# Optimization experiments

Hardware: AMD Instinct MI355X
Metric: run time of the kernel (lower is better)

Reference implementation:

```python
import jax, jax.numpy as jnp
import numpy as np

N = 50000      # nodes
E = 800000     # edges (before self-loops)
F_IN = 128     # num_features
HID = 32       # hidden_channels
HEADS = 4
CLS = 40       # num_classes
NEG_SLOPE = 0.2


def setup_inputs() -> dict:
    key = jax.random.key(0)
    ks = jax.random.split(key, 10)
    s = 0.1
    x = jax.random.normal(ks[0], (N, F_IN), jnp.float32)
    edge_index = jax.random.randint(ks[1], (2, E), 0, N, jnp.int32)
    W1 = jax.random.normal(ks[2], (F_IN, HEADS * HID), jnp.float32) * s
    att_src1 = jax.random.normal(ks[3], (HEADS, HID), jnp.float32) * s
    att_dst1 = jax.random.normal(ks[4], (HEADS, HID), jnp.float32) * s
    b1 = jnp.zeros((HEADS * HID,), jnp.float32)
    W2 = jax.random.normal(ks[5], (HEADS * HID, CLS), jnp.float32) * s
    att_src2 = jax.random.normal(ks[6], (1, CLS), jnp.float32) * s
    att_dst2 = jax.random.normal(ks[7], (1, CLS), jnp.float32) * s
    b2 = jnp.zeros((CLS,), jnp.float32)
    return {"x": x, "edge_index": edge_index,
            "W1": W1, "att_src1": att_src1, "att_dst1": att_dst1, "b1": b1,
            "W2": W2, "att_src2": att_src2, "att_dst2": att_dst2, "b2": b2}


def gat_layer(x, src, dst, W, a_src, a_dst, b, concat):
    """PyG GATConv: per-head linear, edge attention logits a_src.h_j + a_dst.h_i,
    LeakyReLU, segment softmax over incoming edges per dst, weighted scatter-sum."""
    n = x.shape[0]
    H, C = a_src.shape
    h = (x @ W).reshape(n, H, C)                       # [N, H, C]
    al_s = jnp.einsum('nhc,hc->nh', h, a_src)          # [N, H]
    al_d = jnp.einsum('nhc,hc->nh', h, a_dst)          # [N, H]
    e = jax.nn.leaky_relu(al_s[src] + al_d[dst], NEG_SLOPE)  # [E, H]
    e_max = jax.lax.stop_gradient(jax.ops.segment_max(e, dst, num_segments=n))
    e = jnp.exp(e - e_max[dst])
    denom = jax.ops.segment_sum(e, dst, num_segments=n)      # [N, H]
    alpha = e / (denom[dst] + 1e-16)                         # [E, H]
    out = jax.ops.segment_sum(h[src] * alpha[:, :, None], dst, num_segments=n)  # [N, H, C]
    out = out.reshape(n, H * C) if concat else out.mean(axis=1)
    return out + b


def reference(x, edge_index, W1, att_src1, att_dst1, b1, W2, att_src2, att_dst2, b2):
    n = x.shape[0]
    loops = jnp.arange(n, dtype=edge_index.dtype)
    src = jnp.concatenate([edge_index[0], loops])  # PyG adds self-loops by default
    dst = jnp.concatenate([edge_index[1], loops])
    h = gat_layer(x, src, dst, W1, att_src1, att_dst1, b1, concat=True)
    h = jax.nn.relu(h)  # dropout is identity in eval mode
    h = gat_layer(h, src, dst, W2, att_src2, att_dst2, b2, concat=False)
    return jax.nn.log_softmax(h, axis=1)
```

## Files before the change

kernel.cpp:

```cpp
#include <hip/hip_runtime.h>
#include <hip/hip_bf16.h>
#include <cstdint>
#include <cstddef>

#define NN 50000
#define EE 800000
#define ETOT (EE + NN)
#define FIN 128
#define D1 128
#define HEADS 4
#define HID 32
#define CLS 40
#define NEG 0.2f
#define MAXDEG 64
#define NPART 8
#define PSIZE 6250
#define GB 79
#define BGB (NPART * GB)

typedef __attribute__((ext_vector_type(8))) short short8;
typedef __attribute__((ext_vector_type(4))) float float4v;

union U16 { uint4 u; short8 s; };

__device__ __forceinline__ float bf2f(unsigned short u) {
    union { unsigned int i; float f; } v; v.i = ((unsigned int)u) << 16; return v.f;
}
__device__ __forceinline__ unsigned short f2bf(float f) {
    union { unsigned int i; float f; } v; v.f = f;
    unsigned int r = v.i + 0x7fffu + ((v.i >> 16) & 1u);
    return (unsigned short)(r >> 16);
}

__global__ __launch_bounds__(256, 4) void bg_k(const int* __restrict__ eidx,
                                               int* __restrict__ cnt,
                                               unsigned short* __restrict__ ssrcp,
                                               const float* __restrict__ X,
                                               const float* __restrict__ W,
                                               const float* __restrict__ as1,
                                               const float* __restrict__ ad1,
                                               unsigned int* __restrict__ H1b,
                                               float* __restrict__ ALS1,
                                               float* __restrict__ ALD1) {
    __shared__ uint4 Wl[2048];
    __shared__ float sas[128], sad[128];
    int t = threadIdx.x;

    if (blockIdx.x < BGB) {
        int part = blockIdx.x & (NPART - 1);
        int g    = blockIdx.x >> 3;
        int lo = part * PSIZE, hi = lo + PSIZE;
        int stride = GB * 256;
        for (int n = lo + g * 256 + t; n < hi; n += stride) {
            int slot = atomicAdd(&cnt[n], 1);
            if (slot < MAXDEG) ssrcp[n * MAXDEG + slot] = (unsigned short)n;
        }
        const int4* dst4 = (const int4*)(eidx + EE);
        for (int i4 = g * 256 + t; i4 < EE / 4; i4 += stride) {
            int4 d = dst4[i4];
            int base = i4 * 4;
            if (d.x >= lo && d.x < hi) {
                int sN = eidx[base];
                int slot = atomicAdd(&cnt[d.x], 1);
                if (slot < MAXDEG) ssrcp[d.x * MAXDEG + slot] = (unsigned short)sN;
            }
            if (d.y >= lo && d.y < hi) {
                int sN = eidx[base + 1];
                int slot = atomicAdd(&cnt[d.y], 1);
                if (slot < MAXDEG) ssrcp[d.y * MAXDEG + slot] = (unsigned short)sN;
            }
            if (d.z >= lo && d.z < hi) {
                int sN = eidx[base + 2];
                int slot = atomicAdd(&cnt[d.z], 1);
                if (slot < MAXDEG) ssrcp[d.z * MAXDEG + slot] = (unsigned short)sN;
            }
            if (d.w >= lo && d.w < hi) {
                int sN = eidx[base + 3];
                int slot = atomicAdd(&cnt[d.w], 1);
                if (slot < MAXDEG) ssrcp[d.w * MAXDEG + slot] = (unsigned short)sN;
            }
        }
        return;
    }

    int bI = blockIdx.x - BGB;
    if (t < 128) { sas[t] = as1[t]; sad[t] = ad1[t]; }
    for (int g = t; g < 2048; g += 256) {
        int ct = g >> 8, rem = g & 255, kc = rem >> 6, l = rem & 63;
        int c = ct * 16 + (l & 15);
        int k0 = kc * 32 + (l >> 4) * 8;
        U16 u;
#pragma unroll
        for (int j = 0; j < 8; j++) u.s[j] = (short)f2bf(W[(k0 + j) * D1 + c]);
        Wl[g] = u.u;
    }
    __syncthreads();

    int wid = t >> 6, lane = t & 63, quad = lane >> 4, lrow = lane & 15;
    int wrow0 = bI * 128 + wid * 32;

    short8 afr[2][4];
#pragma unroll
    for (int rt = 0; rt < 2; rt++) {
        int r = wrow0 + rt * 16 + lrow;
#pragma unroll
        for (int kc = 0; kc < 4; kc++) {
            short8 a = {0, 0, 0, 0, 0, 0, 0, 0};
            if (r < NN) {
                const float* xp = X + (size_t)r * FIN + kc * 32 + quad * 8;
                float4 x0 = *(const float4*)xp;
                float4 x1 = *(const float4*)(xp + 4);
                a[0] = (short)f2bf(x0.x); a[1] = (short)f2bf(x0.y);
                a[2] = (short)f2bf(x0.z); a[3] = (short)f2bf(x0.w);
                a[4] = (short)f2bf(x1.x); a[5] = (short)f2bf(x1.y);
                a[6] = (short)f2bf(x1.z); a[7] = (short)f2bf(x1.w);
            }
            afr[rt][kc] = a;
        }
    }

    float4v acc[2][4];

    for (int cp = 0; cp < 2; ++cp) {
#pragma unroll
        for (int rt = 0; rt < 2; rt++)
#pragma unroll
            for (int c4 = 0; c4 < 4; c4++) acc[rt][c4] = (float4v)(0.f);

#pragma unroll
        for (int c4 = 0; c4 < 4; c4++) {
#pragma unroll
            for (int kc = 0; kc < 4; kc++) {
                U16 b; b.u = Wl[((cp * 4 + c4) * 4 + kc) * 64 + lane];
                acc[0][c4] = __builtin_amdgcn_mfma_f32_16x16x32_bf16(afr[0][kc], b.s, acc[0][c4], 0, 0, 0);
                acc[1][c4] = __builtin_amdgcn_mfma_f32_16x16x32_bf16(afr[1][kc], b.s, acc[1][c4], 0, 0, 0);
            }
        }

#pragma unroll
        for (int rt = 0; rt < 2; rt++) {
#pragma unroll
            for (int reg = 0; reg < 4; reg++) {
                float ps[2] = {0.f, 0.f};
                float pd[2] = {0.f, 0.f};
#pragma unroll
                for (int c4 = 0; c4 < 4; c4++) {
                    float v = acc[rt][c4][reg];
                    int ct = cp * 4 + c4;
                    ps[c4 >> 1] += v * sas[ct * 16 + lrow];
                    pd[c4 >> 1] += v * sad[ct * 16 + lrow];
                }
#pragma unroll
                for (int o = 1; o < 16; o <<= 1) {
#pragma unroll
                    for (int h = 0; h < 2; h++) {
                        ps[h] += __shfl_xor(ps[h], o);
                        pd[h] += __shfl_xor(pd[h], o);
                    }
                }
                int r = wrow0 + rt * 16 + quad * 4 + reg;
                if (lrow == 0 && r < NN) {
                    *(float2*)&ALS1[(size_t)r * 4 + cp * 2] = make_float2(ps[0], ps[1]);
                    *(float2*)&ALD1[(size_t)r * 4 + cp * 2] = make_float2(pd[0], pd[1]);
                }
            }
        }

#pragma unroll
        for (int rt = 0; rt < 2; rt++)
#pragma unroll
            for (int c4 = 0; c4 < 4; c4++)
#pragma unroll
                for (int reg = 0; reg < 4; reg++) {
                    float v = acc[rt][c4][reg];
                    float o = __shfl_xor(v, 1);
                    int r = wrow0 + rt * 16 + quad * 4 + reg;
                    if (((lane & 1) == 0) && r < NN) {
                        unsigned int u = (unsigned int)f2bf(v) | ((unsigned int)f2bf(o) << 16);
                        H1b[(size_t)r * 64 + (cp * 4 + c4) * 8 + (lrow >> 1)] = u;
                    }
                }
    }
}

__global__ __launch_bounds__(256) void gather1_k(const int* __restrict__ cnt,
                                                 const unsigned short* __restrict__ ssrcp,
                                                 const uint4* __restrict__ H1b4,
                                                 const float4* __restrict__ ALS,
                                                 const float4* __restrict__ ALD,
                                                 const float* __restrict__ b1,
                                                 uint4* __restrict__ OUT1b4) {
    __shared__ float wlds[4][MAXDEG][4];
    __shared__ int sidlds[4][MAXDEG];
    int wid = threadIdx.x >> 6, lane = threadIdx.x & 63;
    int v = blockIdx.x * 4 + wid;
    int deg = min(cnt[v], MAXDEG);
    float4 ad = ALD[v];
    float w0 = 0.f, w1 = 0.f, w2 = 0.f, w3 = 0.f;
    if (lane < deg) {
        int s = (int)ssrcp[v * MAXDEG + lane];
        sidlds[wid][lane] = s;
        float4 as = ALS[s];
        float l0 = as.x + ad.x; l0 = l0 > 0.f ? l0 : NEG * l0;
        float l1 = as.y + ad.y; l1 = l1 > 0.f ? l1 : NEG * l1;
        float l2 = as.z + ad.z; l2 = l2 > 0.f ? l2 : NEG * l2;
        float l3 = as.w + ad.w; l3 = l3 > 0.f ? l3 : NEG * l3;
        w0 = __expf(l0); w1 = __expf(l1); w2 = __expf(l2); w3 = __expf(l3);
        wlds[wid][lane][0] = w0; wlds[wid][lane][1] = w1;
        wlds[wid][lane][2] = w2; wlds[wid][lane][3] = w3;
    }
    float d0 = w0, d1 = w1, d2 = w2, d3 = w3;
#pragma unroll
    for (int o = 1; o < 64; o <<= 1) {
        d0 += __shfl_xor(d0, o); d1 += __shfl_xor(d1, o);
        d2 += __shfl_xor(d2, o); d3 += __shfl_xor(d3, o);
    }
    __syncthreads();
    int g = lane >> 4, l = lane & 15, head = l >> 2;
    float a0=0.f,a1=0.f,a2=0.f,a3=0.f,a4=0.f,a5=0.f,a6=0.f,a7=0.f;
    {
        int j = g;
        bool valid = j < deg;
        float wj = 0.f; uint4 q = {};
        if (valid) {
            wj = wlds[wid][j][head];
            q = H1b4[(size_t)sidlds[wid][j] * 16 + l];
        }
        while (valid) {
            int jn = j + 4;
            bool vn = jn < deg;
            float wn = 0.f; uint4 qn = {};
            if (vn) {
                wn = wlds[wid][jn][head];
                qn = H1b4[(size_t)sidlds[wid][jn] * 16 + l];
            }
            a0 += wj * bf2f((unsigned short)(q.x & 0xffffu));
            a1 += wj * bf2f((unsigned short)(q.x >> 16));
            a2 += wj * bf2f((unsigned short)(q.y & 0xffffu));
            a3 += wj * bf2f((unsigned short)(q.y >> 16));
            a4 += wj * bf2f((unsigned short)(q.z & 0xffffu));
            a5 += wj * bf2f((unsigned short)(q.z >> 16));
            a6 += wj * bf2f((unsigned short)(q.w & 0xffffu));
            a7 += wj * bf2f((unsigned short)(q.w >> 16));
            j = jn; valid = vn; wj = wn; q = qn;
        }
    }
#pragma unroll
    for (int o = 16; o < 64; o <<= 1) {
        a0 += __shfl_xor(a0, o); a1 += __shfl_xor(a1, o);
        a2 += __shfl_xor(a2, o); a3 += __shfl_xor(a3, o);
        a4 += __shfl_xor(a4, o); a5 += __shfl_xor(a5, o);
        a6 += __shfl_xor(a6, o); a7 += __shfl_xor(a7, o);
    }
    if (lane < 16) {
        float den = (head == 0) ? d0 : (head == 1) ? d1 : (head == 2) ? d2 : d3;
        den += 1e-16f;
        float4 bA = *(const float4*)&b1[8 * l];
        float4 bB = *(const float4*)&b1[8 * l + 4];
        float o0 = fmaxf(a0 / den + bA.x, 0.f);
        float o1 = fmaxf(a1 / den + bA.y, 0.f);
        float o2 = fmaxf(a2 / den + bA.z, 0.f);
        float o3 = fmaxf(a3 / den + bA.w, 0.f);
        float o4 = fmaxf(a4 / den + bB.x, 0.f);
        float o5 = fmaxf(a5 / den + bB.y, 0.f);
        float o6 = fmaxf(a6 / den + bB.z, 0.f);
        float o7 = fmaxf(a7 / den + bB.w, 0.f);
        uint4 u;
        u.x = (unsigned int)f2bf(o0) | ((unsigned int)f2bf(o1) << 16);
        u.y = (unsigned int)f2bf(o2) | ((unsigned int)f2bf(o3) << 16);
        u.z = (unsigned int)f2bf(o4) | ((unsigned int)f2bf(o5) << 16);
        u.w = (unsigned int)f2bf(o6) | ((unsigned int)f2bf(o7) << 16);
        OUT1b4[(size_t)v * 16 + l] = u;
    }
}

__global__ __launch_bounds__(256) void gemm2_k(const unsigned int* __restrict__ OUT1b,
                                               const float* __restrict__ W2,
                                               const float* __restrict__ as2,
                                               const float* __restrict__ ad2,
                                               unsigned int* __restrict__ H2b,
                                               float* __restrict__ ALS2,
                                               float* __restrict__ ALD2) {
    __shared__ uint4 Wl[768];
    __shared__ float sas[48], sad[48];
    int t = threadIdx.x;
    if (t < 48) {
        sas[t] = (t < CLS) ? as2[t] : 0.f;
        sad[t] = (t < CLS) ? ad2[t] : 0.f;
    }
    for (int g = t; g < 768; g += 256) {
        int ct = g >> 8, rem = g & 255, kc = rem >> 6, l = rem & 63;
        int c = ct * 16 + (l & 15);
        int k0 = kc * 32 + (l >> 4) * 8;
        U16 u;
#pragma unroll
        for (int j = 0; j < 8; j++)
            u.s[j] = (c < CLS) ? (short)f2bf(W2[(k0 + j) * CLS + c]) : (short)0;
        Wl[g] = u.u;
    }
    __syncthreads();

    int wid = t >> 6, lane = t & 63, quad = lane >> 4, lrow = lane & 15;
    int wrow0 = blockIdx.x * 128 + wid * 32;

    U16 afr[2][4];
#pragma unroll
    for (int rt = 0; rt < 2; rt++) {
        int r = wrow0 + rt * 16 + lrow;
#pragma unroll
        for (int kc = 0; kc < 4; kc++) {
            if (r < NN)
                afr[rt][kc].u = ((const uint4*)OUT1b)[(size_t)r * 16 + kc * 4 + quad];
            else
                afr[rt][kc].u = make_uint4(0, 0, 0, 0);
        }
    }

    float4v acc[2][3];
#pragma unroll
    for (int rt = 0; rt < 2; rt++)
#pragma unroll
        for (int ct = 0; ct < 3; ct++) acc[rt][ct] = (float4v)(0.f);

#pragma unroll
    for (int ct = 0; ct < 3; ct++) {
#pragma unroll
        for (int kc = 0; kc < 4; kc++) {
            U16 b; b.u = Wl[(ct * 4 + kc) * 64 + lane];
            acc[0][ct] = __builtin_amdgcn_mfma_f32_16x16x32_bf16(afr[0][kc].s, b.s, acc[0][ct], 0, 0, 0);
            acc[1][ct] = __builtin_amdgcn_mfma_f32_16x16x32_bf16(afr[1][kc].s, b.s, acc[1][ct], 0, 0, 0);
        }
    }

#pragma unroll
    for (int rt = 0; rt < 2; rt++) {
#pragma unroll
        for (int reg = 0; reg < 4; reg++) {
            float ps = 0.f, pd = 0.f;
#pragma unroll
            for (int ct = 0; ct < 3; ct++) {
                float v = acc[rt][ct][reg];
                ps += v * sas[ct * 16 + lrow];
                pd += v * sad[ct * 16 + lrow];
            }
#pragma unroll
            for (int o = 1; o < 16; o <<= 1) {
                ps += __shfl_xor(ps, o);
                pd += __shfl_xor(pd, o);
            }
            int r = wrow0 + rt * 16 + quad * 4 + reg;
            if (lrow == 0 && r < NN) {
                ALS2[r] = ps;
                ALD2[r] = pd;
            }
        }
    }

#pragma unroll
    for (int rt = 0; rt < 2; rt++)
#pragma unroll
        for (int ct = 0; ct < 3; ct++)
#pragma unroll
            for (int reg = 0; reg < 4; reg++) {
                float v = acc[rt][ct][reg];
                float o = __shfl_xor(v, 1);
                int r = wrow0 + rt * 16 + quad * 4 + reg;
                int c = ct * 16 + lrow;
                if (((lane & 1) == 0) && c < CLS && r < NN) {
                    unsigned int u = (unsigned int)f2bf(v) | ((unsigned int)f2bf(o) << 16);
                    H2b[(size_t)r * 20 + (c >> 1)] = u;
                }
            }
}

__global__ __launch_bounds__(256) void gather2_k(const int* __restrict__ cnt,
                                                 const unsigned short* __restrict__ ssrcp,
                                                 const unsigned int* __restrict__ H2b,
                                                 const float* __restrict__ ALS,
                                                 const float* __restrict__ ALD,
                                                 const float* __restrict__ b2,
                                                 float* __restrict__ out) {
    int wid = threadIdx.x >> 6, t = threadIdx.x & 63;
    int v = blockIdx.x * 4 + wid;
    int deg = min(cnt[v], MAXDEG);
    __shared__ float w[4][MAXDEG];
    __shared__ int sid[4][MAXDEG];
    __shared__ float part[4][3][CLS];
    float den = 0.f;
    float adv = ALD[v];
    if (t < deg) {
        int s = (int)ssrcp[(size_t)v * MAXDEG + t];
        sid[wid][t] = s;
        float l = ALS[s] + adv; l = l > 0.f ? l : NEG * l;
        float e = __expf(l);
        w[wid][t] = e; den = e;
    }
    __syncthreads();
    int g = t / 20, c = t % 20;
    if (t < 60) {
        float ax = 0.f, ay = 0.f;
        int j = g;
        bool valid = j < deg;
        float wj = 0.f; unsigned int u = 0u;
        if (valid) { wj = w[wid][j]; u = H2b[(size_t)sid[wid][j] * 20 + c]; }
        while (valid) {
            int jn = j + 3;
            bool vn = jn < deg;
            float wn = 0.f; unsigned int un = 0u;
            if (vn) { wn = w[wid][jn]; un = H2b[(size_t)sid[wid][jn] * 20 + c]; }
            ax += wj * bf2f((unsigned short)(u & 0xffffu));
            ay += wj * bf2f((unsigned short)(u >> 16));
            j = jn; valid = vn; wj = wn; u = un;
        }
        part[wid][g][2 * c] = ax;
        part[wid][g][2 * c + 1] = ay;
    }
#pragma unroll
    for (int o = 32; o > 0; o >>= 1) den += __shfl_xor(den, o);
    __syncthreads();
    float z = (t < CLS) ? (part[wid][0][t] + part[wid][1][t] + part[wid][2][t]) / (den + 1e-16f) + b2[t]
                        : -1e30f;
    float mx = z;
#pragma unroll
    for (int o = 32; o > 0; o >>= 1) mx = fmaxf(mx, __shfl_xor(mx, o));
    float ex = (t < CLS) ? __expf(z - mx) : 0.f;
    float se = ex;
#pragma unroll
    for (int o = 32; o > 0; o >>= 1) se += __shfl_xor(se, o);
    if (t < CLS) out[(size_t)v * CLS + t] = z - mx - __logf(se);
}

extern "C" void kernel_launch(void* const* d_in, const int* in_sizes, int n_in,
                              void* d_out, int out_size, void* d_ws, size_t ws_size,
                              hipStream_t stream) {
    const float* x   = (const float*)d_in[0];
    const int*   eix = (const int*)d_in[1];
    const float* W1  = (const float*)d_in[2];
    const float* as1 = (const float*)d_in[3];
    const float* ad1 = (const float*)d_in[4];
    const float* b1  = (const float*)d_in[5];
    const float* W2  = (const float*)d_in[6];
    const float* as2 = (const float*)d_in[7];
    const float* ad2 = (const float*)d_in[8];
    const float* b2  = (const float*)d_in[9];
    float* out = (float*)d_out;

    char* p = (char*)d_ws;
    auto carve = [&](size_t bytes) -> void* {
        void* r = (void*)p;
        p += (bytes + 255) & ~(size_t)255;
        return r;
    };
    unsigned int* H1b   = (unsigned int*)carve((size_t)NN * 64 * 4);
    unsigned int* OUT1b = (unsigned int*)carve((size_t)NN * 64 * 4);
    unsigned int* H2b   = (unsigned int*)carve((size_t)NN * 20 * 4);
    float* ALS1 = (float*)carve((size_t)NN * 4 * 4);
    float* ALD1 = (float*)carve((size_t)NN * 4 * 4);
    float* ALS2 = (float*)carve((size_t)NN * 4);
    float* ALD2 = (float*)carve((size_t)NN * 4);
    int* cnt    = (int*)carve((size_t)NN * 4);
    unsigned short* ssrcp = (unsigned short*)carve((size_t)NN * MAXDEG * 2);

    hipMemsetAsync(cnt, 0, (size_t)NN * 4, stream);

    int gemmBlocks = (NN + 127) / 128;
    bg_k<<<BGB + gemmBlocks, 256, 0, stream>>>(eix, cnt, ssrcp, x, W1, as1, ad1,
                                               H1b, ALS1, ALD1);
    gather1_k<<<NN / 4, 256, 0, stream>>>(cnt, ssrcp, (const uint4*)H1b,
                                          (const float4*)ALS1, (const float4*)ALD1,
                                          b1, (uint4*)OUT1b);
    gemm2_k<<<(NN + 127) / 128, 256, 0, stream>>>(OUT1b, W2, as2, ad2, H2b, ALS2, ALD2);
    gather2_k<<<NN / 4, 256, 0, stream>>>(cnt, ssrcp, H2b, ALS2, ALD2, b2, out);
}
```

Before: 219.4 us.

## Fuse all GAT stages into one persistent kernel with grid barriers

Replaces the memset plus four separate kernel launches with a single persistent kernel. The kernel is sized from the occupancy query, hardcodes 256 CUs, and moves between phases through a hierarchical software grid barrier built on atomics and a monotonically increasing flag. Work is spread with grid-stride loops over node tasks, and the memset is replaced by in-kernel zeroing of the counts. This removes launch gaps and tail effects between stages. In exchange, every block waits at each barrier, occupancy is limited, and correctness depends on all blocks being co-resident.

```diff
diff --git a/kernel.cpp b/kernel.cpp
--- a/kernel.cpp
+++ b/kernel.cpp
@@ -1,11 +1,9 @@
 #include <hip/hip_runtime.h>
-#include <hip/hip_bf16.h>
 #include <cstdint>
 #include <cstddef>
 
 #define NN 50000
 #define EE 800000
-#define ETOT (EE + NN)
 #define FIN 128
 #define D1 128
 #define HEADS 4
@@ -13,10 +11,8 @@
 #define CLS 40
 #define NEG 0.2f
 #define MAXDEG 64
-#define NPART 8
-#define PSIZE 6250
-#define GB 79
-#define BGB (NPART * GB)
+#define NT 12500
+#define GEMM1T 391
 
 typedef __attribute__((ext_vector_type(8))) short short8;
 typedef __attribute__((ext_vector_type(4))) float float4v;
@@ -32,402 +28,438 @@
     return (unsigned short)(r >> 16);
 }
 
-__global__ __launch_bounds__(256, 4) void bg_k(const int* __restrict__ eidx,
-                                               int* __restrict__ cnt,
-                                               unsigned short* __restrict__ ssrcp,
-                                               const float* __restrict__ X,
-                                               const float* __restrict__ W,
-                                               const float* __restrict__ as1,
-                                               const float* __restrict__ ad1,
-                                               unsigned int* __restrict__ H1b,
-                                               float* __restrict__ ALS1,
-                                               float* __restrict__ ALD1) {
-    __shared__ uint4 Wl[2048];
-    __shared__ float sas[128], sad[128];
+__device__ int g_gcnt[32 * 16];
+__device__ int g_root;
+__device__ unsigned long long g_flag;
+
+__device__ __forceinline__ void spin_until(unsigned long long tgt) {
+    while (__hip_atomic_load(&g_flag, __ATOMIC_RELAXED, __HIP_MEMORY_SCOPE_AGENT) < tgt)
+        __builtin_amdgcn_s_sleep(2);
+    (void)__hip_atomic_load(&g_flag, __ATOMIC_ACQUIRE, __HIP_MEMORY_SCOPE_AGENT);
+}
+
+__device__ __forceinline__ void grid_barrier(int k, unsigned long long base, int nblocks) {
+    __syncthreads();
+    if (threadIdx.x == 0) {
+        unsigned long long tgt = base + (unsigned long long)k;
+        int grp  = blockIdx.x >> 5;
+        int ngrp = (nblocks + 31) >> 5;
+        int gsz  = min(32, nblocks - grp * 32);
+        int a = __hip_atomic_fetch_add(&g_gcnt[grp * 16], 1, __ATOMIC_ACQ_REL, __HIP_MEMORY_SCOPE_AGENT);
+        if (a == gsz - 1) {
+            __hip_atomic_store(&g_gcnt[grp * 16], 0, __ATOMIC_RELAXED, __HIP_MEMORY_SCOPE_AGENT);
+            int r = __hip_atomic_fetch_add(&g_root, 1, __ATOMIC_ACQ_REL, __HIP_MEMORY_SCOPE_AGENT);
+            if (r == ngrp - 1) {
+                __hip_atomic_store(&g_root, 0, __ATOMIC_RELAXED, __HIP_MEMORY_SCOPE_AGENT);
+                __hip_atomic_store(&g_flag, tgt, __ATOMIC_RELEASE, __HIP_MEMORY_SCOPE_AGENT);
+            } else spin_until(tgt);
+        } else spin_until(tgt);
+    }
+    __syncthreads();
+}
+
+struct P1S { uint4 Wl[2048]; float sas[128]; float sad[128]; };
+struct G1S { float wlds[4][MAXDEG][4]; int sidlds[4][MAXDEG]; };
+struct P3S { uint4 Wl[768]; float sas[48]; float sad[48]; };
+struct G2S { float w[4][MAXDEG]; int sid[4][MAXDEG]; float part[4][3][CLS]; };
+union SMEM { P1S p1; G1S g1; P3S p3; G2S g2; };
+
+__global__ __launch_bounds__(256, 4) void mega_k(const int* __restrict__ eidx,
+                                                 int* __restrict__ cnt,
+                                                 unsigned short* __restrict__ ssrcp,
+                                                 const float* __restrict__ X,
+                                                 const float* __restrict__ W1,
+                                                 const float* __restrict__ as1,
+                                                 const float* __restrict__ ad1,
+                                                 unsigned int* __restrict__ H1b,
+                                                 float* __restrict__ ALS1,
+                                                 float* __restrict__ ALD1,
+                                                 const float* __restrict__ b1,
+                                                 uint4* __restrict__ OUT1b4,
+                                                 const float* __restrict__ W2,
+                                                 const float* __restrict__ as2,
+                                                 const float* __restrict__ ad2,
+                                                 unsigned int* __restrict__ H2b,
+                                                 float* __restrict__ ALS2,
+                                                 float* __restrict__ ALD2,
+                                                 const float* __restrict__ b2,
+                                                 float* __restrict__ out,
+                                                 int nblocks, int buildB) {
+    __shared__ SMEM sm;
     int t = threadIdx.x;
 
-    if (blockIdx.x < BGB) {
-        int part = blockIdx.x & (NPART - 1);
+    unsigned long long base = 0;
+    if (t == 0) base = __hip_atomic_load(&g_flag, __ATOMIC_ACQUIRE, __HIP_MEMORY_SCOPE_AGENT);
+
+    for (int i = blockIdx.x * 256 + t; i < NN; i += nblocks * 256)
+        __hip_atomic_store(&cnt[i], 0, __ATOMIC_RELAXED, __HIP_MEMORY_SCOPE_AGENT);
+
+    grid_barrier(1, base, nblocks);
+
+    if (blockIdx.x < buildB) {
+        int part = blockIdx.x & 7;
         int g    = blockIdx.x >> 3;
-        int lo = part * PSIZE, hi = lo + PSIZE;
-        int stride = GB * 256;
+        int GBd  = buildB >> 3;
+        int lo = part * (NN / 8), hi = lo + (NN / 8);
+        int stride = GBd * 256;
         for (int n = lo + g * 256 + t; n < hi; n += stride) {
             int slot = atomicAdd(&cnt[n], 1);
-            if (slot < MAXDEG) ssrcp[n * MAXDEG + slot] = (unsigned short)n;
+            if (slot < MAXDEG) ssrcp[(size_t)n * MAXDEG + slot] = (unsigned short)n;
         }
         const int4* dst4 = (const int4*)(eidx + EE);
         for (int i4 = g * 256 + t; i4 < EE / 4; i4 += stride) {
             int4 d = dst4[i4];
-            int base = i4 * 4;
+            int bgi = i4 * 4;
             if (d.x >= lo && d.x < hi) {
-                int sN = eidx[base];
+                int sN = eidx[bgi];
                 int slot = atomicAdd(&cnt[d.x], 1);
-                if (slot < MAXDEG) ssrcp[d.x * MAXDEG + slot] = (unsigned short)sN;
+                if (slot < MAXDEG) ssrcp[(size_t)d.x * MAXDEG + slot] = (unsigned short)sN;
             }
             if (d.y >= lo && d.y < hi) {
-                int sN = eidx[base + 1];
+                int sN = eidx[bgi + 1];
                 int slot = atomicAdd(&cnt[d.y], 1);
-                if (slot < MAXDEG) ssrcp[d.y * MAXDEG + slot] = (unsigned short)sN;
+                if (slot < MAXDEG) ssrcp[(size_t)d.y * MAXDEG + slot] = (unsigned short)sN;
             }
             if (d.z >= lo && d.z < hi) {
-                int sN = eidx[base + 2];
+                int sN = eidx[bgi + 2];
                 int slot = atomicAdd(&cnt[d.z], 1);
-                if (slot < MAXDEG) ssrcp[d.z * MAXDEG + slot] = (unsigned short)sN;
+                if (slot < MAXDEG) ssrcp[(size_t)d.z * MAXDEG + slot] = (unsigned short)sN;
             }
             if (d.w >= lo && d.w < hi) {
-                int sN = eidx[base + 3];
+                int sN = eidx[bgi + 3];
                 int slot = atomicAdd(&cnt[d.w], 1);
-                if (slot < MAXDEG) ssrcp[d.w * MAXDEG + slot] = (unsigned short)sN;
-            }
-        }
-        return;
+                if (slot < MAXDEG) ssrcp[(size_t)d.w * MAXDEG + slot] = (unsigned short)sN;
+            }
+        }
+    } else {
+        if (t < 128) { sm.p1.sas[t] = as1[t]; sm.p1.sad[t] = ad1[t]; }
+        for (int g = t; g < 2048; g += 256) {
+            int ct = g >> 8, rem = g & 255, kc = rem >> 6, l = rem & 63;
+            int c = ct * 16 + (l & 15);
+            int k0 = kc * 32 + (l >> 4) * 8;
+            U16 u;
+#pragma unroll
+            for (int j = 0; j < 8; j++) u.s[j] = (short)f2bf(W1[(k0 + j) * D1 + c]);
+            sm.p1.Wl[g] = u.u;
+        }
+        __syncthreads();
+
+        int wid = t >> 6, lane = t & 63, quad = lane >> 4, lrow = lane & 15;
+        int gspan = nblocks - buildB;
+        for (int bI = blockIdx.x - buildB; bI < GEMM1T; bI += gspan) {
+            int wrow0 = bI * 128 + wid * 32;
+            short8 afr[2][4];
+#pragma unroll
+            for (int rt = 0; rt < 2; rt++) {
+                int r = wrow0 + rt * 16 + lrow;
+#pragma unroll
+                for (int kc = 0; kc < 4; kc++) {
+                    short8 a = {0, 0, 0, 0, 0, 0, 0, 0};
+                    if (r < NN) {
+                        const float* xp = X + (size_t)r * FIN + kc * 32 + quad * 8;
+                        float4 x0 = *(const float4*)xp;
+                        float4 x1 = *(const float4*)(xp + 4);
+                        a[0] = (short)f2bf(x0.x); a[1] = (short)f2bf(x0.y);
+                        a[2] = (short)f2bf(x0.z); a[3] = (short)f2bf(x0.w);
+                        a[4] = (short)f2bf(x1.x); a[5] = (short)f2bf(x1.y);
+                        a[6] = (short)f2bf(x1.z); a[7] = (short)f2bf(x1.w);
+                    }
+                    afr[rt][kc] = a;
+                }
+            }
+
+            float4v acc[2][4];
+            for (int cp = 0; cp < 2; ++cp) {
+#pragma unroll
+                for (int rt = 0; rt < 2; rt++)
+#pragma unroll
+                    for (int c4 = 0; c4 < 4; c4++) acc[rt][c4] = (float4v)(0.f);
+#pragma unroll
+                for (int c4 = 0; c4 < 4; c4++) {
+#pragma unroll
+                    for (int kc = 0; kc < 4; kc++) {
+                        U16 b; b.u = sm.p1.Wl[((cp * 4 + c4) * 4 + kc) * 64 + lane];
+                        acc[0][c4] = __builtin_amdgcn_mfma_f32_16x16x32_bf16(afr[0][kc], b.s, acc[0][c4], 0, 0, 0);
+                        acc[1][c4] = __builtin_amdgcn_mfma_f32_16x16x32_bf16(afr[1][kc], b.s, acc[1][c4], 0, 0, 0);
+                    }
+                }
+#pragma unroll
+                for (int rt = 0; rt < 2; rt++) {
+#pragma unroll
+                    for (int reg = 0; reg < 4; reg++) {
+                        float ps[2] = {0.f, 0.f};
+                        float pd[2] = {0.f, 0.f};
+#pragma unroll
+                        for (int c4 = 0; c4 < 4; c4++) {
+                            float v = acc[rt][c4][reg];
+                            int ct = cp * 4 + c4;
+                            ps[c4 >> 1] += v * sm.p1.sas[ct * 16 + lrow];
+                            pd[c4 >> 1] += v * sm.p1.sad[ct * 16 + lrow];
+                        }
+#pragma unroll
+                        for (int o = 1; o < 16; o <<= 1) {
+#pragma unroll
+                            for (int h = 0; h < 2; h++) {
+                                ps[h] += __shfl_xor(ps[h], o);
+                                pd[h] += __shfl_xor(pd[h], o);
+                            }
+                        }
+                        int r = wrow0 + rt * 16 + quad * 4 + reg;
+                        if (lrow == 0 && r < NN) {
+                            *(float2*)&ALS1[(size_t)r * 4 + cp * 2] = make_float2(ps[0], ps[1]);
+                            *(float2*)&ALD1[(size_t)r * 4 + cp * 2] = make_float2(pd[0], pd[1]);
+                        }
+                    }
+                }
+#pragma unroll
+                for (int rt = 0; rt < 2; rt++)
+#pragma unroll
+                    for (int c4 = 0; c4 < 4; c4++)
+#pragma unroll
+                        for (int reg = 0; reg < 4; reg++) {
+                            float v = acc[rt][c4][reg];
+                            float o = __shfl_xor(v, 1);
+                            int r = wrow0 + rt * 16 + quad * 4 + reg;
+                            if (((lane & 1) == 0) && r < NN) {
+                                unsigned int u = (unsigned int)f2bf(v) | ((unsigned int)f2bf(o) << 16);
+                                H1b[(size_t)r * 64 + (cp * 4 + c4) * 8 + (lrow >> 1)] = u;
+                            }
+                        }
+            }
+        }
     }
 
-    int bI = blockIdx.x - BGB;
-    if (t < 128) { sas[t] = as1[t]; sad[t] = ad1[t]; }
-    for (int g = t; g < 2048; g += 256) {
-        int ct = g >> 8, rem = g & 255, kc = rem >> 6, l = rem & 63;
-        int c = ct * 16 + (l & 15);
-        int k0 = kc * 32 + (l >> 4) * 8;
-        U16 u;
-#pragma unroll
-        for (int j = 0; j < 8; j++) u.s[j] = (short)f2bf(W[(k0 + j) * D1 + c]);
-        Wl[g] = u.u;
+    grid_barrier(2, base, nblocks);
+
+    {
+        const uint4* H1b4 = (const uint4*)H1b;
+        int wid = t >> 6, lane = t & 63;
+        for (int task = blockIdx.x; task < NT; task += nblocks) {
+            int v = task * 4 + wid;
+            int deg = min(cnt[v], MAXDEG);
+            float4 ad = *(const float4*)&ALD1[(size_t)v * 4];
+            float w0 = 0.f, w1 = 0.f, w2 = 0.f, w3 = 0.f;
+            if (lane < deg) {
+                int s = (int)ssrcp[(size_t)v * MAXDEG + lane];
+                sm.g1.sidlds[wid][lane] = s;
+                float4 as = *(const float4*)&ALS1[(size_t)s * 4];
+                float l0 = as.x + ad.x; l0 = l0 > 0.f ? l0 : NEG * l0;
+                float l1 = as.y + ad.y; l1 = l1 > 0.f ? l1 : NEG * l1;
+                float l2 = as.z + ad.z; l2 = l2 > 0.f ? l2 : NEG * l2;
+                float l3 = as.w + ad.w; l3 = l3 > 0.f ? l3 : NEG * l3;
+                w0 = __expf(l0); w1 = __expf(l1); w2 = __expf(l2); w3 = __expf(l3);
+                sm.g1.wlds[wid][lane][0] = w0; sm.g1.wlds[wid][lane][1] = w1;
+                sm.g1.wlds[wid][lane][2] = w2; sm.g1.wlds[wid][lane][3] = w3;
+            }
+            float d0 = w0, d1 = w1, d2 = w2, d3 = w3;
+#pragma unroll
+            for (int o = 1; o < 64; o <<= 1) {
+                d0 += __shfl_xor(d0, o); d1 += __shfl_xor(d1, o);
+                d2 += __shfl_xor(d2, o); d3 += __shfl_xor(d3, o);
+            }
+            __syncthreads();
+            int g = lane >> 4, l = lane & 15, head = l >> 2;
+            float a0=0.f,a1=0.f,a2=0.f,a3=0.f,a4=0.f,a5=0.f,a6=0.f,a7=0.f;
+            {
+                int j = g;
+                bool valid = j < deg;
+                float wj = 0.f; uint4 q = {};
+                if (valid) {
+                    wj = sm.g1.wlds[wid][j][head];
+                    q = H1b4[(size_t)sm.g1.sidlds[wid][j] * 16 + l];
+                }
+                while (valid) {
+                    int jn = j + 4;
+                    bool vn = jn < deg;
+                    float wn = 0.f; uint4 qn = {};
+                    if (vn) {
+                        wn = sm.g1.wlds[wid][jn][head];
+                        qn = H1b4[(size_t)sm.g1.sidlds[wid][jn] * 16 + l];
+                    }
+                    a0 += wj * bf2f((unsigned short)(q.x & 0xffffu));
+                    a1 += wj * bf2f((unsigned short)(q.x >> 16));
+                    a2 += wj * bf2f((unsigned short)(q.y & 0xffffu));
+                    a3 += wj * bf2f((unsigned short)(q.y >> 16));
+                    a4 += wj * bf2f((unsigned short)(q.z & 0xffffu));
+                    a5 += wj * bf2f((unsigned short)(q.z >> 16));
+                    a6 += wj * bf2f((unsigned short)(q.w & 0xffffu));
+                    a7 += wj * bf2f((unsigned short)(q.w >> 16));
+                    j = jn; valid = vn; wj = wn; q = qn;
+                }
+            }
+#pragma unroll
+            for (int o = 16; o < 64; o <<= 1) {
+                a0 += __shfl_xor(a0, o); a1 += __shfl_xor(a1, o);
+                a2 += __shfl_xor(a2, o); a3 += __shfl_xor(a3, o);
+                a4 += __shfl_xor(a4, o); a5 += __shfl_xor(a5, o);
+                a6 += __shfl_xor(a6, o); a7 += __shfl_xor(a7, o);
+            }
+            if (lane < 16) {
+                float den = (head == 0) ? d0 : (head == 1) ? d1 : (head == 2) ? d2 : d3;
+                den += 1e-16f;
+                float4 bA = *(const float4*)&b1[8 * l];
+                float4 bB = *(const float4*)&b1[8 * l + 4];
+                float o0 = fmaxf(a0 / den + bA.x, 0.f);
+                float o1 = fmaxf(a1 / den + bA.y, 0.f);
+                float o2 = fmaxf(a2 / den + bA.z, 0.f);
+                float o3 = fmaxf(a3 / den + bA.w, 0.f);
+                float o4 = fmaxf(a4 / den + bB.x, 0.f);
+                float o5 = fmaxf(a5 / den + bB.y, 0.f);
+                float o6 = fmaxf(a6 / den + bB.z, 0.f);
+                float o7 = fmaxf(a7 / den + bB.w, 0.f);
+                uint4 u;
+                u.x = (unsigned int)f2bf(o0) | ((unsigned int)f2bf(o1) << 16);
+                u.y = (unsigned int)f2bf(o2) | ((unsigned int)f2bf(o3) << 16);
+                u.z = (unsigned int)f2bf(o4) | ((unsigned int)f2bf(o5) << 16);
+                u.w = (unsigned int)f2bf(o6) | ((unsigned int)f2bf(o7) << 16);
+                OUT1b4[(size_t)v * 16 + l] = u;
+            }
+            __syncthreads();
+        }
     }
-    __syncthreads();
-
-    int wid = t >> 6, lane = t & 63, quad = lane >> 4, lrow = lane & 15;
-    int wrow0 = bI * 128 + wid * 32;
-
-    short8 afr[2][4];
-#pragma unroll
-    for (int rt = 0; rt < 2; rt++) {
-        int r = wrow0 + rt * 16 + lrow;
-#pragma unroll
-        for (int kc = 0; kc < 4; kc++) {
-            short8 a = {0, 0, 0, 0, 0, 0, 0, 0};
-            if (r < NN) {
-                const float* xp = X + (size_t)r * FIN + kc * 32 + quad * 8;
-                float4 x0 = *(const float4*)xp;
-                float4 x1 = *(const float4*)(xp + 4);
-                a[0] = (short)f2bf(x0.x); a[1] = (short)f2bf(x0.y);
-                a[2] = (short)f2bf(x0.z); a[3] = (short)f2bf(x0.w);
-                a[4] = (short)f2bf(x1.x); a[5] = (short)f2bf(x1.y);
-                a[6] = (short)f2bf(x1.z); a[7] = (short)f2bf(x1.w);
-            }
-            afr[rt][kc] = a;
+
+    grid_barrier(3, base, nblocks);
+
+    {
+        if (t < 48) {
+            sm.p3.sas[t] = (t < CLS) ? as2[t] : 0.f;
+            sm.p3.sad[t] = (t < CLS) ? ad2[t] : 0.f;
+        }
+        for (int g = t; g < 768; g += 256) {
+            int ct = g >> 8, rem = g & 255, kc = rem >> 6, l = rem & 63;
+            int c = ct * 16 + (l & 15);
+            int k0 = kc * 32 + (l >> 4) * 8;
+            U16 u;
+#pragma unroll
+            for (int j = 0; j < 8; j++)
+                u.s[j] = (c < CLS) ? (short)f2bf(W2[(k0 + j) * CLS + c]) : (short)0;
+            sm.p3.Wl[g] = u.u;
+        }
+        __syncthreads();
+
+        int wid = t >> 6, lane = t & 63, quad = lane >> 4, lrow = lane & 15;
+        for (int bI = blockIdx.x; bI < GEMM1T; bI += nblocks) {
+            int wrow0 = bI * 128 + wid * 32;
+            U16 afr[2][4];
+#pragma unroll
+            for (int rt = 0; rt < 2; rt++) {
+                int r = wrow0 + rt * 16 + lrow;
+#pragma unroll
+                for (int kc = 0; kc < 4; kc++) {
+                    if (r < NN)
+                        afr[rt][kc].u = OUT1b4[(size_t)r * 16 + kc * 4 + quad];
+                    else
+                        afr[rt][kc].u = make_uint4(0, 0, 0, 0);
+                }
+            }
+            float4v acc[2][3];
+#pragma unroll
+            for (int rt = 0; rt < 2; rt++)
+#pragma unroll
+                for (int ct = 0; ct < 3; ct++) acc[rt][ct] = (float4v)(0.f);
+#pragma unroll
+            for (int ct = 0; ct < 3; ct++) {
+#pragma unroll
+                for (int kc = 0; kc < 4; kc++) {
+                    U16 b; b.u = sm.p3.Wl[(ct * 4 + kc) * 64 + lane];
+                    acc[0][ct] = __builtin_amdgcn_mfma_f32_16x16x32_bf16(afr[0][kc].s, b.s, acc[0][ct], 0, 0, 0);
+                    acc[1][ct] = __builtin_amdgcn_mfma_f32_16x16x32_bf16(afr[1][kc].s, b.s, acc[1][ct], 0, 0, 0);
+                }
+            }
+#pragma unroll
+            for (int rt = 0; rt < 2; rt++) {
+#pragma unroll
+                for (int reg = 0; reg < 4; reg++) {
+                    float ps = 0.f, pd = 0.f;
+#pragma unroll
+                    for (int ct = 0; ct < 3; ct++) {
+                        float v = acc[rt][ct][reg];
+                        ps += v * sm.p3.sas[ct * 16 + lrow];
+                        pd += v * sm.p3.sad[ct * 16 + lrow];
+                    }
+#pragma unroll
+                    for (int o = 1; o < 16; o <<= 1) {
+                        ps += __shfl_xor(ps, o);
+                        pd += __shfl_xor(pd, o);
+                    }
+                    int r = wrow0 + rt * 16 + quad * 4 + reg;
+                    if (lrow == 0 && r < NN) {
+                        ALS2[r] = ps;
+                        ALD2[r] = pd;
+                    }
+                }
+            }
+#pragma unroll
+            for (int rt = 0; rt < 2; rt++)
+#pragma unroll
+                for (int ct = 0; ct < 3; ct++)
+#pragma unroll
+                    for (int reg = 0; reg < 4; reg++) {
+                        float v = acc[rt][ct][reg];
+                        float o = __shfl_xor(v, 1);
+                        int r = wrow0 + rt * 16 + quad * 4 + reg;
+                        int c = ct * 16 + lrow;
+                        if (((lane & 1) == 0) && c < CLS && r < NN) {
+                            unsigned int u = (unsigned int)f2bf(v) | ((unsigned int)f2bf(o) << 16);
+                            H2b[(size_t)r * 20 + (c >> 1)] = u;
+                        }
+                    }
         }
     }
 
-    float4v acc[2][4];
-
-    for (int cp = 0; cp < 2; ++cp) {
-#pragma unroll
-        for (int rt = 0; rt < 2; rt++)
-#pragma unroll
-            for (int c4 = 0; c4 < 4; c4++) acc[rt][c4] = (float4v)(0.f);
-
-#pragma unroll
-        for (int c4 = 0; c4 < 4; c4++) {
-#pragma unroll
-            for (int kc = 0; kc < 4; kc++) {
-                U16 b; b.u = Wl[((cp * 4 + c4) * 4 + kc) * 64 + lane];
-                acc[0][c4] = __builtin_amdgcn_mfma_f32_16x16x32_bf16(afr[0][kc], b.s, acc[0][c4], 0, 0, 0);
-                acc[1][c4] = __builtin_amdgcn_mfma_f32_16x16x32_bf16(afr[1][kc], b.s, acc[1][c4], 0, 0, 0);
-            }
-        }
-
-#pragma unroll
-        for (int rt = 0; rt < 2; rt++) {
-#pragma unroll
-            for (int reg = 0; reg < 4; reg++) {
-                float ps[2] = {0.f, 0.f};
-                float pd[2] = {0.f, 0.f};
-#pragma unroll
-                for (int c4 = 0; c4 < 4; c4++) {
-                    float v = acc[rt][c4][reg];
-                    int ct = cp * 4 + c4;
-                    ps[c4 >> 1] += v * sas[ct * 16 + lrow];
-                    pd[c4 >> 1] += v * sad[ct * 16 + lrow];
-                }
-#pragma unroll
-                for (int o = 1; o < 16; o <<= 1) {
-#pragma unroll
-                    for (int h = 0; h < 2; h++) {
-                        ps[h] += __shfl_xor(ps[h], o);
-                        pd[h] += __shfl_xor(pd[h], o);
-                    }
-                }
-                int r = wrow0 + rt * 16 + quad * 4 + reg;
-                if (lrow == 0 && r < NN) {
-                    *(float2*)&ALS1[(size_t)r * 4 + cp * 2] = make_float2(ps[0], ps[1]);
-                    *(float2*)&ALD1[(size_t)r * 4 + cp * 2] = make_float2(pd[0], pd[1]);
-                }
-            }
-        }
-
-#pragma unroll
-        for (int rt = 0; rt < 2; rt++)
-#pragma unroll
-            for (int c4 = 0; c4 < 4; c4++)
-#pragma unroll
-                for (int reg = 0; reg < 4; reg++) {
-                    float v = acc[rt][c4][reg];
-                    float o = __shfl_xor(v, 1);
-                    int r = wrow0 + rt * 16 + quad * 4 + reg;
-                    if (((lane & 1) == 0) && r < NN) {
-                        unsigned int u = (unsigned int)f2bf(v) | ((unsigned int)f2bf(o) << 16);
-                        H1b[(size_t)r * 64 + (cp * 4 + c4) * 8 + (lrow >> 1)] = u;
-                    }
-                }
+    grid_barrier(4, base, nblocks);
+
+    {
+        int wid = t >> 6, lt = t & 63;
+        for (int task = blockIdx.x; task < NT; task += nblocks) {
+            int v = task * 4 + wid;
+            int deg = min(cnt[v], MAXDEG);
+            float den = 0.f;
+            float adv = ALD2[v];
+            if (lt < deg) {
+                int s = (int)ssrcp[(size_t)v * MAXDEG + lt];
+                sm.g2.sid[wid][lt] = s;
+                float l = ALS2[s] + adv; l = l > 0.f ? l : NEG * l;
+                float e = __expf(l);
+                sm.g2.w[wid][lt] = e; den = e;
+            }
+            __syncthreads();
+            int g = lt / 20, c = lt % 20;
+            if (lt < 60) {
+                float ax = 0.f, ay = 0.f;
+                int j = g;
+                bool valid = j < deg;
+                float wj = 0.f; unsigned int u = 0u;
+                if (valid) { wj = sm.g2.w[wid][j]; u = H2b[(size_t)sm.g2.sid[wid][j] * 20 + c]; }
+                while (valid) {
+                    int jn = j + 3;
+                    bool vn = jn < deg;
+                    float wn = 0.f; unsigned int un = 0u;
+                    if (vn) { wn = sm.g2.w[wid][jn]; un = H2b[(size_t)sm.g2.sid[wid][jn] * 20 + c]; }
+                    ax += wj * bf2f((unsigned short)(u & 0xffffu));
+                    ay += wj * bf2f((unsigned short)(u >> 16));
+                    j = jn; valid = vn; wj = wn; u = un;
+                }
+                sm.g2.part[wid][g][2 * c] = ax;
+                sm.g2.part[wid][g][2 * c + 1] = ay;
+            }
+#pragma unroll
+            for (int o = 32; o > 0; o >>= 1) den += __shfl_xor(den, o);
+            __syncthreads();
+            float z = (lt < CLS) ? (sm.g2.part[wid][0][lt] + sm.g2.part[wid][1][lt] + sm.g2.part[wid][2][lt])
+                                        / (den + 1e-16f) + b2[lt]
+                                 : -1e30f;
+            float mx = z;
+#pragma unroll
+            for (int o = 32; o > 0; o >>= 1) mx = fmaxf(mx, __shfl_xor(mx, o));
+            float ex = (lt < CLS) ? __expf(z - mx) : 0.f;
+            float se = ex;
+#pragma unroll
+            for (int o = 32; o > 0; o >>= 1) se += __shfl_xor(se, o);
+            if (lt < CLS) out[(size_t)v * CLS + lt] = z - mx - __logf(se);
+            __syncthreads();
+        }
     }
-}
-
-__global__ __launch_bounds__(256) void gather1_k(const int* __restrict__ cnt,
-                                                 const unsigned short* __restrict__ ssrcp,
-                                                 const uint4* __restrict__ H1b4,
-                                                 const float4* __restrict__ ALS,
-                                                 const float4* __restrict__ ALD,
-                                                 const float* __restrict__ b1,
-                                                 uint4* __restrict__ OUT1b4) {
-    __shared__ float wlds[4][MAXDEG][4];
-    __shared__ int sidlds[4][MAXDEG];
-    int wid = threadIdx.x >> 6, lane = threadIdx.x & 63;
-    int v = blockIdx.x * 4 + wid;
-    int deg = min(cnt[v], MAXDEG);
-    float4 ad = ALD[v];
-    float w0 = 0.f, w1 = 0.f, w2 = 0.f, w3 = 0.f;
-    if (lane < deg) {
-        int s = (int)ssrcp[v * MAXDEG + lane];
-        sidlds[wid][lane] = s;
-        float4 as = ALS[s];
-        float l0 = as.x + ad.x; l0 = l0 > 0.f ? l0 : NEG * l0;
-        float l1 = as.y + ad.y; l1 = l1 > 0.f ? l1 : NEG * l1;
-        float l2 = as.z + ad.z; l2 = l2 > 0.f ? l2 : NEG * l2;
-        float l3 = as.w + ad.w; l3 = l3 > 0.f ? l3 : NEG * l3;
-        w0 = __expf(l0); w1 = __expf(l1); w2 = __expf(l2); w3 = __expf(l3);
-        wlds[wid][lane][0] = w0; wlds[wid][lane][1] = w1;
-        wlds[wid][lane][2] = w2; wlds[wid][lane][3] = w3;
-    }
-    float d0 = w0, d1 = w1, d2 = w2, d3 = w3;
-#pragma unroll
-    for (int o = 1; o < 64; o <<= 1) {
-        d0 += __shfl_xor(d0, o); d1 += __shfl_xor(d1, o);
-        d2 += __shfl_xor(d2, o); d3 += __shfl_xor(d3, o);
-    }
-    __syncthreads();
-    int g = lane >> 4, l = lane & 15, head = l >> 2;
-    float a0=0.f,a1=0.f,a2=0.f,a3=0.f,a4=0.f,a5=0.f,a6=0.f,a7=0.f;
-    {
-        int j = g;
-        bool valid = j < deg;
-        float wj = 0.f; uint4 q = {};
-        if (valid) {
-            wj = wlds[wid][j][head];
-            q = H1b4[(size_t)sidlds[wid][j] * 16 + l];
-        }
-        while (valid) {
-            int jn = j + 4;
-            bool vn = jn < deg;
-            float wn = 0.f; uint4 qn = {};
-            if (vn) {
-                wn = wlds[wid][jn][head];
-                qn = H1b4[(size_t)sidlds[wid][jn] * 16 + l];
-            }
-            a0 += wj * bf2f((unsigned short)(q.x & 0xffffu));
-            a1 += wj * bf2f((unsigned short)(q.x >> 16));
-            a2 += wj * bf2f((unsigned short)(q.y & 0xffffu));
-            a3 += wj * bf2f((unsigned short)(q.y >> 16));
-            a4 += wj * bf2f((unsigned short)(q.z & 0xffffu));
-            a5 += wj * bf2f((unsigned short)(q.z >> 16));
-            a6 += wj * bf2f((unsigned short)(q.w & 0xffffu));
-            a7 += wj * bf2f((unsigned short)(q.w >> 16));
-            j = jn; valid = vn; wj = wn; q = qn;
-        }
-    }
-#pragma unroll
-    for (int o = 16; o < 64; o <<= 1) {
-        a0 += __shfl_xor(a0, o); a1 += __shfl_xor(a1, o);
-        a2 += __shfl_xor(a2, o); a3 += __shfl_xor(a3, o);
-        a4 += __shfl_xor(a4, o); a5 += __shfl_xor(a5, o);
-        a6 += __shfl_xor(a6, o); a7 += __shfl_xor(a7, o);
-    }
-    if (lane < 16) {
-        float den = (head == 0) ? d0 : (head == 1) ? d1 : (head == 2) ? d2 : d3;
-        den += 1e-16f;
-        float4 bA = *(const float4*)&b1[8 * l];
-        float4 bB = *(const float4*)&b1[8 * l + 4];
-        float o0 = fmaxf(a0 / den + bA.x, 0.f);
-        float o1 = fmaxf(a1 / den + bA.y, 0.f);
-        float o2 = fmaxf(a2 / den + bA.z, 0.f);
-        float o3 = fmaxf(a3 / den + bA.w, 0.f);
-        float o4 = fmaxf(a4 / den + bB.x, 0.f);
-        float o5 = fmaxf(a5 / den + bB.y, 0.f);
-        float o6 = fmaxf(a6 / den + bB.z, 0.f);
-        float o7 = fmaxf(a7 / den + bB.w, 0.f);
-        uint4 u;
-        u.x = (unsigned int)f2bf(o0) | ((unsigned int)f2bf(o1) << 16);
-        u.y = (unsigned int)f2bf(o2) | ((unsigned int)f2bf(o3) << 16);
-        u.z = (unsigned int)f2bf(o4) | ((unsigned int)f2bf(o5) << 16);
-        u.w = (unsigned int)f2bf(o6) | ((unsigned int)f2bf(o7) << 16);
-        OUT1b4[(size_t)v * 16 + l] = u;
-    }
-}
-
-__global__ __launch_bounds__(256) void gemm2_k(const unsigned int* __restrict__ OUT1b,
-                                               const float* __restrict__ W2,
-                                               const float* __restrict__ as2,
-                                               const float* __restrict__ ad2,
-                                               unsigned int* __restrict__ H2b,
-                                               float* __restrict__ ALS2,
-                                               float* __restrict__ ALD2) {
-    __shared__ uint4 Wl[768];
-    __shared__ float sas[48], sad[48];
-    int t = threadIdx.x;
-    if (t < 48) {
-        sas[t] = (t < CLS) ? as2[t] : 0.f;
-        sad[t] = (t < CLS) ? ad2[t] : 0.f;
-    }
-    for (int g = t; g < 768; g += 256) {
-        int ct = g >> 8, rem = g & 255, kc = rem >> 6, l = rem & 63;
-        int c = ct * 16 + (l & 15);
-        int k0 = kc * 32 + (l >> 4) * 8;
-        U16 u;
-#pragma unroll
-        for (int j = 0; j < 8; j++)
-            u.s[j] = (c < CLS) ? (short)f2bf(W2[(k0 + j) * CLS + c]) : (short)0;
-        Wl[g] = u.u;
-    }
-    __syncthreads();
-
-    int wid = t >> 6, lane = t & 63, quad = lane >> 4, lrow = lane & 15;
-    int wrow0 = blockIdx.x * 128 + wid * 32;
-
-    U16 afr[2][4];
-#pragma unroll
-    for (int rt = 0; rt < 2; rt++) {
-        int r = wrow0 + rt * 16 + lrow;
-#pragma unroll
-        for (int kc = 0; kc < 4; kc++) {
-            if (r < NN)
-                afr[rt][kc].u = ((const uint4*)OUT1b)[(size_t)r * 16 + kc * 4 + quad];
-            else
-                afr[rt][kc].u = make_uint4(0, 0, 0, 0);
-        }
-    }
-
-    float4v acc[2][3];
-#pragma unroll
-    for (int rt = 0; rt < 2; rt++)
-#pragma unroll
-        for (int ct = 0; ct < 3; ct++) acc[rt][ct] = (float4v)(0.f);
-
-#pragma unroll
-    for (int ct = 0; ct < 3; ct++) {
-#pragma unroll
-        for (int kc = 0; kc < 4; kc++) {
-            U16 b; b.u = Wl[(ct * 4 + kc) * 64 + lane];
-            acc[0][ct] = __builtin_amdgcn_mfma_f32_16x16x32_bf16(afr[0][kc].s, b.s, acc[0][ct], 0, 0, 0);
-            acc[1][ct] = __builtin_amdgcn_mfma_f32_16x16x32_bf16(afr[1][kc].s, b.s, acc[1][ct], 0, 0, 0);
-        }
-    }
-
-#pragma unroll
-    for (int rt = 0; rt < 2; rt++) {
-#pragma unroll
-        for (int reg = 0; reg < 4; reg++) {
-            float ps = 0.f, pd = 0.f;
-#pragma unroll
-            for (int ct = 0; ct < 3; ct++) {
-                float v = acc[rt][ct][reg];
-                ps += v * sas[ct * 16 + lrow];
-                pd += v * sad[ct * 16 + lrow];
-            }
-#pragma unroll
-            for (int o = 1; o < 16; o <<= 1) {
-                ps += __shfl_xor(ps, o);
-                pd += __shfl_xor(pd, o);
-            }
-            int r = wrow0 + rt * 16 + quad * 4 + reg;
-            if (lrow == 0 && r < NN) {
-                ALS2[r] = ps;
-                ALD2[r] = pd;
-            }
-        }
-    }
-
-#pragma unroll
-    for (int rt = 0; rt < 2; rt++)
-#pragma unroll
-        for (int ct = 0; ct < 3; ct++)
-#pragma unroll
-            for (int reg = 0; reg < 4; reg++) {
-                float v = acc[rt][ct][reg];
-                float o = __shfl_xor(v, 1);
-                int r = wrow0 + rt * 16 + quad * 4 + reg;
-                int c = ct * 16 + lrow;
-                if (((lane & 1) == 0) && c < CLS && r < NN) {
-                    unsigned int u = (unsigned int)f2bf(v) | ((unsigned int)f2bf(o) << 16);
-                    H2b[(size_t)r * 20 + (c >> 1)] = u;
-                }
-            }
-}
-
-__global__ __launch_bounds__(256) void gather2_k(const int* __restrict__ cnt,
-                                                 const unsigned short* __restrict__ ssrcp,
-                                                 const unsigned int* __restrict__ H2b,
-                                                 const float* __restrict__ ALS,
-                                                 const float* __restrict__ ALD,
-                                                 const float* __restrict__ b2,
-                                                 float* __restrict__ out) {
-    int wid = threadIdx.x >> 6, t = threadIdx.x & 63;
-    int v = blockIdx.x * 4 + wid;
-    int deg = min(cnt[v], MAXDEG);
-    __shared__ float w[4][MAXDEG];
-    __shared__ int sid[4][MAXDEG];
-    __shared__ float part[4][3][CLS];
-    float den = 0.f;
-    float adv = ALD[v];
-    if (t < deg) {
-        int s = (int)ssrcp[(size_t)v * MAXDEG + t];
-        sid[wid][t] = s;
-        float l = ALS[s] + adv; l = l > 0.f ? l : NEG * l;
-        float e = __expf(l);
-        w[wid][t] = e; den = e;
-    }
-    __syncthreads();
-    int g = t / 20, c = t % 20;
-    if (t < 60) {
-        float ax = 0.f, ay = 0.f;
-        int j = g;
-        bool valid = j < deg;
-        float wj = 0.f; unsigned int u = 0u;
-        if (valid) { wj = w[wid][j]; u = H2b[(size_t)sid[wid][j] * 20 + c]; }
-        while (valid) {
-            int jn = j + 3;
-            bool vn = jn < deg;
-            float wn = 0.f; unsigned int un = 0u;
-            if (vn) { wn = w[wid][jn]; un = H2b[(size_t)sid[wid][jn] * 20 + c]; }
-            ax += wj * bf2f((unsigned short)(u & 0xffffu));
-            ay += wj * bf2f((unsigned short)(u >> 16));
-            j = jn; valid = vn; wj = wn; u = un;
-        }
-        part[wid][g][2 * c] = ax;
-        part[wid][g][2 * c + 1] = ay;
-    }
-#pragma unroll
-    for (int o = 32; o > 0; o >>= 1) den += __shfl_xor(den, o);
-    __syncthreads();
-    float z = (t < CLS) ? (part[wid][0][t] + part[wid][1][t] + part[wid][2][t]) / (den + 1e-16f) + b2[t]
-                        : -1e30f;
-    float mx = z;
-#pragma unroll
-    for (int o = 32; o > 0; o >>= 1) mx = fmaxf(mx, __shfl_xor(mx, o));
-    float ex = (t < CLS) ? __expf(z - mx) : 0.f;
-    float se = ex;
-#pragma unroll
-    for (int o = 32; o > 0; o >>= 1) se += __shfl_xor(se, o);
-    if (t < CLS) out[(size_t)v * CLS + t] = z - mx - __logf(se);
 }
 
 extern "C" void kernel_launch(void* const* d_in, const int* in_sizes, int n_in,
@@ -461,14 +493,21 @@
     int* cnt    = (int*)carve((size_t)NN * 4);
     unsigned short* ssrcp = (unsigned short*)carve((size_t)NN * MAXDEG * 2);
 
-    hipMemsetAsync(cnt, 0, (size_t)NN * 4, stream);
-
-    int gemmBlocks = (NN + 127) / 128;
-    bg_k<<<BGB + gemmBlocks, 256, 0, stream>>>(eix, cnt, ssrcp, x, W1, as1, ad1,
-                                               H1b, ALS1, ALD1);
-    gather1_k<<<NN / 4, 256, 0, stream>>>(cnt, ssrcp, (const uint4*)H1b,
-                                          (const float4*)ALS1, (const float4*)ALD1,
-                                          b1, (uint4*)OUT1b);
-    gemm2_k<<<(NN + 127) / 128, 256, 0, stream>>>(OUT1b, W2, as2, ad2, H2b, ALS2, ALD2);
-    gather2_k<<<NN / 4, 256, 0, stream>>>(cnt, ssrcp, H2b, ALS2, ALD2, b2, out);
+    static int s_nb = 0;
+    if (s_nb == 0) {
+        int occ = 0;
+        hipError_t e = hipOccupancyMaxActiveBlocksPerMultiprocessor(&occ, mega_k, 256, 0);
+        if (e != hipSuccess || occ < 1) occ = 1;
+        if (occ > 4) occ = 4;
+        s_nb = occ * 256;
+    }
+    int nb = s_nb;
+    int buildB = ((nb * 632 / 1024) / 8) * 8;
+    if (buildB < 8) buildB = 8;
+    if (nb - buildB < 8) buildB = nb - 8;
+
+    mega_k<<<nb, 256, 0, stream>>>(eix, cnt, ssrcp, x, W1, as1, ad1,
+                                   H1b, ALS1, ALD1, b1, (uint4*)OUT1b,
+                                   W2, as2, ad2, H2b, ALS2, ALD2, b2, out,
+                                   nb, buildB);
 }
```

New measurement: 436.1 us. 98.8% more time.
